# Optimization experiments

Measured on AMD Instinct MI355X. Metric: run time of the kernel, lower is better.

The kernel has to match this reference:

```python
import jax, jax.numpy as jnp
import numpy as np

E, M, K, N = 8, 32768, 1024, 1024


def setup_inputs() -> dict:
    key = jax.random.key(0)
    ks = jax.random.split(key, 5)
    # int8-valued activations/weights stored as int32 (spec has no int8)
    x = jax.random.randint(ks[0], (M, K), -128, 128, dtype=jnp.int32)
    weight = jax.random.randint(ks[1], (E, K, N), -128, 128, dtype=jnp.int32)
    # dequant scales: per-expert-per-channel and per-token
    scale = jax.random.uniform(ks[2], (E, N), dtype=jnp.float32) * 0.01
    per_token_scale = jax.random.uniform(ks[3], (M,), dtype=jnp.float32) * 0.01
    # group_list_type == 0 -> cumulative end offsets per expert, last == M
    cuts = jnp.sort(jax.random.randint(ks[4], (E - 1,), 0, M))
    group_list = jnp.concatenate([cuts, jnp.array([M])]).astype(jnp.int64)
    return {
        "x": x,
        "weight": weight,
        "scale": scale,
        "per_token_scale": per_token_scale,
        "group_list": group_list,
        "group_list_type": 0,
        "output_dtype": 0,
    }


def reference(x, weight, scale, per_token_scale, group_list, group_list_type, output_dtype):
    # cumulative group boundaries (end offsets per expert)
    cum = group_list if group_list_type == 0 else jnp.cumsum(group_list)
    m = x.shape[0]
    # expert id for each token: token t belongs to expert e iff cum[e-1] <= t < cum[e]
    eid = jnp.searchsorted(cum, jnp.arange(m), side="right")  # [M]
    xf = x.astype(jnp.float32)
    acc = jnp.zeros((m, weight.shape[2]), jnp.float32)  # int32 accumulator in fp32
    # dense-fallback grouped GEMM: mask tokens per expert, one GEMM per expert
    for e in range(weight.shape[0]):
        mask = (eid == e).astype(jnp.float32)[:, None]
        acc = acc + (xf * mask) @ weight[e].astype(jnp.float32)
    # fused dequant: per-expert-per-channel scale * per-token scale
    y = acc * scale[eid] * per_token_scale[:, None]
    return y.astype(jnp.float32)  # output_dtype 0 -> float32
```

## Files before the change

### kernel.cpp

```cpp
#include <hip/hip_runtime.h>

#define M_DIM 32768
#define K_DIM 1024
#define N_DIM 1024
#define E_NUM 8

#define BM 128
#define BN 128
#define BK 128
#define KSTEPS (K_DIM / BK)

typedef __attribute__((ext_vector_type(4))) int v4i;

__global__ __launch_bounds__(256) void pack_x_kernel(const int4* __restrict__ x,
                                                     int4* __restrict__ xq) {
    const int i = blockIdx.x * 256 + threadIdx.x;
    int4 a = x[i * 4 + 0], b = x[i * 4 + 1], c = x[i * 4 + 2], d = x[i * 4 + 3];
    int4 o;
    o.x = (a.x & 255) | ((a.y & 255) << 8) | ((a.z & 255) << 16) | (a.w << 24);
    o.y = (b.x & 255) | ((b.y & 255) << 8) | ((b.z & 255) << 16) | (b.w << 24);
    o.z = (c.x & 255) | ((c.y & 255) << 8) | ((c.z & 255) << 16) | (c.w << 24);
    o.w = (d.x & 255) | ((d.y & 255) << 8) | ((d.z & 255) << 16) | (d.w << 24);
    xq[i] = o;
}

__global__ __launch_bounds__(256) void pack_wt_kernel(const int* __restrict__ w,
                                                      int* __restrict__ wt) {
    __shared__ signed char tile[64][260];
    const int e    = blockIdx.z;
    const int n0   = blockIdx.x * 64;
    const int k0   = blockIdx.y * 256;
    const int tid  = threadIdx.x;
    const int lane = tid & 63;
    const int wv   = tid >> 6;

    const int* wp = w + ((size_t)e << 20);
#pragma unroll 4
    for (int i = 0; i < 64; ++i) {
        const int k = wv * 64 + i;
        tile[lane][k] = (signed char)wp[(size_t)(k0 + k) * N_DIM + n0 + lane];
    }
    __syncthreads();

    int* wo = wt + ((size_t)e << 18);
#pragma unroll
    for (int i = 0; i < 16; ++i) {
        const int n = i * 4 + wv;
        const int v = *(const int*)&tile[n][lane * 4];
        wo[(size_t)(n0 + n) * (K_DIM / 4) + (k0 >> 2) + lane] = v;
    }
}

__global__ __launch_bounds__(256, 2) void gmm_kernel(
    const signed char* __restrict__ xq,
    const signed char* __restrict__ wtq,
    const float* __restrict__ scale,
    const float* __restrict__ pts,
    const int* __restrict__ g32,
    float* __restrict__ out)
{
    __shared__ signed char As[2][BM * BK];
    __shared__ signed char Bs[2][BN * BK];

    const int tid  = threadIdx.x;
    const int lane = tid & 63;
    const int wv   = tid >> 6;
    const int gid  = blockIdx.x;
    const int m0   = (gid >> 3) * BM;
    const int n0   = (gid & 7) * BN;

    const bool g_is_i64 = (g32[7] != M_DIM);
    int cum[E_NUM];
#pragma unroll
    for (int e = 0; e < E_NUM; ++e)
        cum[e] = g_is_i64 ? g32[2 * e] : g32[e];
    int e0 = 0;
    while (e0 < E_NUM - 1 && cum[e0] <= m0) ++e0;
    int e1 = 0;
    while (e1 < E_NUM - 1 && cum[e1] <= m0 + BM - 1) ++e1;

    const int wm    = (wv >> 1) * 64;
    const int wn    = (wv & 1) * 64;
    const int row_a = lane & 15;
    const int quad  = lane >> 4;
    const int rx    = row_a & 7;

    const int st_r = lane >> 3;
    const int st_c = ((lane & 7) ^ st_r) * 16;

    const signed char* xg = xq + (size_t)m0 * K_DIM;

    for (int e = e0; e <= e1; ++e) {
        const int lo = (e == 0) ? 0 : cum[e - 1];
        const int hi = cum[e];
        if (hi <= lo) continue;
        const int slo = lo > m0 ? lo : m0;
        const int shi = hi < m0 + BM ? hi : m0 + BM;
        if (slo >= shi) continue;

        const signed char* wg = wtq + ((size_t)e << 20) + (size_t)n0 * K_DIM;

        float sc[4], pt[16];
#pragma unroll
        for (int j = 0; j < 4; ++j)
            sc[j] = scale[e * N_DIM + n0 + wn + j * 16 + row_a];
#pragma unroll
        for (int i = 0; i < 4; ++i)
#pragma unroll
            for (int r = 0; r < 4; ++r)
                pt[i * 4 + r] = pts[m0 + wm + i * 16 + quad * 4 + r];

        v4i acc[4][4];
#pragma unroll
        for (int i = 0; i < 4; ++i)
#pragma unroll
            for (int j = 0; j < 4; ++j)
                acc[i][j] = (v4i){0, 0, 0, 0};

        auto stage = [&](int t, int b) {
            const int kb = t * BK;
#pragma unroll
            for (int s = 0; s < 4; ++s) {
                const int c   = s * 4 + wv;
                const int row = c * 8 + st_r;
                __builtin_amdgcn_global_load_lds(
                    (const __attribute__((address_space(1))) void*)
                        (xg + (size_t)row * K_DIM + kb + st_c),
                    (__attribute__((address_space(3))) void*)(&As[b][c * 1024]),
                    16, 0, 0);
                __builtin_amdgcn_global_load_lds(
                    (const __attribute__((address_space(1))) void*)
                        (wg + (size_t)row * K_DIM + kb + st_c),
                    (__attribute__((address_space(3))) void*)(&Bs[b][c * 1024]),
                    16, 0, 0);
            }
        };

        stage(0, 0);
        __syncthreads();

        for (int t = 0; t < KSTEPS; ++t) {
            const int cur = t & 1;
            if (t + 1 < KSTEPS) stage(t + 1, cur ^ 1);

#pragma unroll
            for (int w = 0; w < 2; ++w) {
                const int sa = ((w << 2) + quad) ^ rx;
                v4i af[4], bf[4];
#pragma unroll
                for (int i = 0; i < 4; ++i)
                    af[i] = *(const v4i*)(&As[cur][(wm + i * 16 + row_a) * BK + sa * 16]);
#pragma unroll
                for (int j = 0; j < 4; ++j)
                    bf[j] = *(const v4i*)(&Bs[cur][(wn + j * 16 + row_a) * BK + sa * 16]);
#pragma unroll
                for (int i = 0; i < 4; ++i)
#pragma unroll
                    for (int j = 0; j < 4; ++j)
                        acc[i][j] = __builtin_amdgcn_mfma_i32_16x16x64_i8(
                            af[i], bf[j], acc[i][j], 0, 0, 0);
            }
            __syncthreads();
        }

#pragma unroll
        for (int i = 0; i < 4; ++i) {
            const int rb = m0 + wm + i * 16 + quad * 4;
#pragma unroll
            for (int j = 0; j < 4; ++j) {
                const int c = n0 + wn + j * 16 + row_a;
#pragma unroll
                for (int r = 0; r < 4; ++r) {
                    const int rr = rb + r;
                    if (rr >= slo && rr < shi)
                        out[(size_t)rr * N_DIM + c] =
                            (float)acc[i][j][r] * sc[j] * pt[i * 4 + r];
                }
            }
        }
    }
}

extern "C" void kernel_launch(void* const* d_in, const int* in_sizes, int n_in,
                              void* d_out, int out_size, void* d_ws, size_t ws_size,
                              hipStream_t stream) {
    const int*   x     = (const int*)d_in[0];
    const int*   w     = (const int*)d_in[1];
    const float* scale = (const float*)d_in[2];
    const float* pts   = (const float*)d_in[3];
    const int*   g32   = (const int*)d_in[4];
    float*       out   = (float*)d_out;

    signed char* xq  = (signed char*)d_ws;
    signed char* wtq = xq + (size_t)M_DIM * K_DIM;

    pack_x_kernel<<<M_DIM * K_DIM / 16 / 256, 256, 0, stream>>>(
        (const int4*)x, (int4*)xq);

    pack_wt_kernel<<<dim3(N_DIM / 64, K_DIM / 256, E_NUM), 256, 0, stream>>>(
        w, (int*)wtq);

    gmm_kernel<<<(M_DIM / BM) * (N_DIM / BN), 256, 0, stream>>>(
        xq, wtq, scale, pts, g32, out);
}
```

Measured before the change: 334.9 us.

## Stage GEMM epilogue through LDS for float4 stores and merge pack kernels

Two changes. The two packing kernels are merged into one launch, with the block index choosing between x packing and weight transposition, which saves one launch and lets the two jobs overlap. The GEMM epilogue now writes the scaled results into shared memory that reuses the operand buffers, synchronises, and then writes coalesced float4 rows to global memory instead of scattered 4-byte stores. This costs two extra barriers per expert segment and an LDS round trip in exchange for better output write efficiency.

```diff
diff --git a/kernel.cpp b/kernel.cpp
--- a/kernel.cpp
+++ b/kernel.cpp
@@ -12,25 +12,29 @@
 
 typedef __attribute__((ext_vector_type(4))) int v4i;
 
-__global__ __launch_bounds__(256) void pack_x_kernel(const int4* __restrict__ x,
-                                                     int4* __restrict__ xq) {
-    const int i = blockIdx.x * 256 + threadIdx.x;
-    int4 a = x[i * 4 + 0], b = x[i * 4 + 1], c = x[i * 4 + 2], d = x[i * 4 + 3];
-    int4 o;
-    o.x = (a.x & 255) | ((a.y & 255) << 8) | ((a.z & 255) << 16) | (a.w << 24);
-    o.y = (b.x & 255) | ((b.y & 255) << 8) | ((b.z & 255) << 16) | (b.w << 24);
-    o.z = (c.x & 255) | ((c.y & 255) << 8) | ((c.z & 255) << 16) | (c.w << 24);
-    o.w = (d.x & 255) | ((d.y & 255) << 8) | ((d.z & 255) << 16) | (d.w << 24);
-    xq[i] = o;
-}
-
-__global__ __launch_bounds__(256) void pack_wt_kernel(const int* __restrict__ w,
-                                                      int* __restrict__ wt) {
+__global__ __launch_bounds__(256) void pack_kernel(const int4* __restrict__ x,
+                                                   int4* __restrict__ xq,
+                                                   const int* __restrict__ w,
+                                                   int* __restrict__ wt) {
     __shared__ signed char tile[64][260];
-    const int e    = blockIdx.z;
-    const int n0   = blockIdx.x * 64;
-    const int k0   = blockIdx.y * 256;
-    const int tid  = threadIdx.x;
+    const int tid = threadIdx.x;
+
+    if (blockIdx.x < 8192) {
+        const int i = blockIdx.x * 256 + tid;
+        int4 a = x[i * 4 + 0], b = x[i * 4 + 1], c = x[i * 4 + 2], d = x[i * 4 + 3];
+        int4 o;
+        o.x = (a.x & 255) | ((a.y & 255) << 8) | ((a.z & 255) << 16) | (a.w << 24);
+        o.y = (b.x & 255) | ((b.y & 255) << 8) | ((b.z & 255) << 16) | (b.w << 24);
+        o.z = (c.x & 255) | ((c.y & 255) << 8) | ((c.z & 255) << 16) | (c.w << 24);
+        o.w = (d.x & 255) | ((d.y & 255) << 8) | ((d.z & 255) << 16) | (d.w << 24);
+        xq[i] = o;
+        return;
+    }
+
+    const int b    = blockIdx.x - 8192;
+    const int e    = b >> 6;
+    const int k0   = ((b >> 4) & 3) * 256;
+    const int n0   = (b & 15) * 64;
     const int lane = tid & 63;
     const int wv   = tid >> 6;
 
@@ -59,8 +63,10 @@
     const int* __restrict__ g32,
     float* __restrict__ out)
 {
-    __shared__ signed char As[2][BM * BK];
-    __shared__ signed char Bs[2][BN * BK];
+    __shared__ signed char smem[4 * BM * BK];
+    signed char* As = smem;
+    signed char* Bs = smem + 2 * BM * BK;
+    float* obuf = (float*)smem;
 
     const int tid  = threadIdx.x;
     const int lane = tid & 63;
@@ -126,12 +132,12 @@
                 __builtin_amdgcn_global_load_lds(
                     (const __attribute__((address_space(1))) void*)
                         (xg + (size_t)row * K_DIM + kb + st_c),
-                    (__attribute__((address_space(3))) void*)(&As[b][c * 1024]),
+                    (__attribute__((address_space(3))) void*)(As + b * BM * BK + c * 1024),
                     16, 0, 0);
                 __builtin_amdgcn_global_load_lds(
                     (const __attribute__((address_space(1))) void*)
                         (wg + (size_t)row * K_DIM + kb + st_c),
-                    (__attribute__((address_space(3))) void*)(&Bs[b][c * 1024]),
+                    (__attribute__((address_space(3))) void*)(Bs + b * BM * BK + c * 1024),
                     16, 0, 0);
             }
         };
@@ -149,10 +155,10 @@
                 v4i af[4], bf[4];
 #pragma unroll
                 for (int i = 0; i < 4; ++i)
-                    af[i] = *(const v4i*)(&As[cur][(wm + i * 16 + row_a) * BK + sa * 16]);
+                    af[i] = *(const v4i*)(As + cur * BM * BK + (wm + i * 16 + row_a) * BK + sa * 16);
 #pragma unroll
                 for (int j = 0; j < 4; ++j)
-                    bf[j] = *(const v4i*)(&Bs[cur][(wn + j * 16 + row_a) * BK + sa * 16]);
+                    bf[j] = *(const v4i*)(Bs + cur * BM * BK + (wn + j * 16 + row_a) * BK + sa * 16);
 #pragma unroll
                 for (int i = 0; i < 4; ++i)
 #pragma unroll
@@ -164,20 +170,26 @@
         }
 
 #pragma unroll
-        for (int i = 0; i < 4; ++i) {
-            const int rb = m0 + wm + i * 16 + quad * 4;
-#pragma unroll
-            for (int j = 0; j < 4; ++j) {
-                const int c = n0 + wn + j * 16 + row_a;
-#pragma unroll
-                for (int r = 0; r < 4; ++r) {
-                    const int rr = rb + r;
-                    if (rr >= slo && rr < shi)
-                        out[(size_t)rr * N_DIM + c] =
-                            (float)acc[i][j][r] * sc[j] * pt[i * 4 + r];
-                }
-            }
+        for (int i = 0; i < 4; ++i)
+#pragma unroll
+            for (int j = 0; j < 4; ++j)
+#pragma unroll
+                for (int r = 0; r < 4; ++r)
+                    obuf[(wm + i * 16 + quad * 4 + r) * BN + wn + j * 16 + row_a] =
+                        (float)acc[i][j][r] * sc[j] * pt[i * 4 + r];
+        __syncthreads();
+
+        const int c4 = (tid & 31) * 4;
+        const int r8 = tid >> 5;
+#pragma unroll
+        for (int it = 0; it < 16; ++it) {
+            const int row = it * 8 + r8;
+            const int rr  = m0 + row;
+            if (rr >= slo && rr < shi)
+                *(float4*)(out + (size_t)rr * N_DIM + n0 + c4) =
+                    *(const float4*)(obuf + row * BN + c4);
         }
+        __syncthreads();
     }
 }
 
@@ -194,11 +206,8 @@
     signed char* xq  = (signed char*)d_ws;
     signed char* wtq = xq + (size_t)M_DIM * K_DIM;
 
-    pack_x_kernel<<<M_DIM * K_DIM / 16 / 256, 256, 0, stream>>>(
-        (const int4*)x, (int4*)xq);
-
-    pack_wt_kernel<<<dim3(N_DIM / 64, K_DIM / 256, E_NUM), 256, 0, stream>>>(
-        w, (int*)wtq);
+    pack_kernel<<<8192 + 512, 256, 0, stream>>>(
+        (const int4*)x, (int4*)xq, w, (int*)wtq);
 
     gmm_kernel<<<(M_DIM / BM) * (N_DIM / BN), 256, 0, stream>>>(
         xq, wtq, scale, pts, g32, out);
```

Measured after the change: 343.6 us. 1.03x slower.
